# Kernel tuning notes

Measured on AMD Instinct MI355X. Metric: run time of the kernel, lower is better.

The kernel has to match this reference:

```python
import jax, jax.numpy as jnp
import numpy as np

EDGES = [[0,1],[0,2],[1,3],[2,3],[1,4],[1,5],[3,5],[4,6],[5,6],[5,27],[5,7],[7,27],[27,26],[26,29],[29,28],[26,28],[26,24],[24,25],[5,8],[8,10],[8,9],[5,9],[9,20],[20,21],[9,16],[15,16],[3,11],[11,12],[11,17],[11,15],[17,18],[18,19],[9,19],[9,23],[11,13],[13,14],[14,22],[22,23],[23,24]]
N_NODES = 30
B = 131072


def setup_inputs() -> dict:
    key = jax.random.key(0)
    ks = jax.random.split(key, 9)
    edge_index = jnp.asarray(np.array(EDGES).T, dtype=jnp.int64)  # [2, 39]
    def glorot(k, shape):
        fan_in = shape[0]
        return jax.random.normal(k, shape, dtype=jnp.float32) / np.sqrt(fan_in)
    return {
        'obs': jax.random.normal(ks[0], (B, N_NODES), dtype=jnp.float32),
        'edge_index': edge_index,
        'w1_rel': glorot(ks[1], (1, 16)),
        'b1_rel': jnp.zeros((16,), dtype=jnp.float32),
        'w1_root': glorot(ks[2], (1, 16)),
        'w2_rel': glorot(ks[3], (16, 1)),
        'b2_rel': jnp.zeros((1,), dtype=jnp.float32),
        'w2_root': glorot(ks[4], (16, 1)),
        'fc_w': glorot(ks[5], (30, 12)),
        'fc_b': jnp.zeros((12,), dtype=jnp.float32),
    }


def graph_conv(x, src, dst, w_rel, b_rel, w_root):
    # x: [B, N, F_in]; scatter-add messages from src nodes into dst nodes
    agg = jnp.zeros_like(x).at[:, dst, :].add(x[:, src, :])  # [B, N, F_in]
    return agg @ w_rel + b_rel + x @ w_root  # [B, N, F_out]


def reference(obs, edge_index, w1_rel, b1_rel, w1_root, w2_rel, b2_rel, w2_root, fc_w, fc_b):
    src, dst = edge_index[0], edge_index[1]
    x = obs.reshape(-1, N_NODES, 1)                    # [B, 30, 1]
    x = jax.nn.sigmoid(graph_conv(x, src, dst, w1_rel, b1_rel, w1_root))  # [B, 30, 16]
    x = jax.nn.sigmoid(graph_conv(x, src, dst, w2_rel, b2_rel, w2_root))  # [B, 30, 1]
    x = x.reshape(-1, N_NODES)                         # [B, 30]
    x = x @ fc_w + fc_b                                # [B, 12]
    x = x.reshape(-1, 2)                               # [B*6, 2]
    return jax.nn.softmax(x, axis=1)
```

## Files before the change

### kernel.cpp

```cpp
#include <hip/hip_runtime.h>

#define LOG2E 1.44269504088896340736f

__device__ __forceinline__ float ex2(float x) { return __builtin_amdgcn_exp2f(x); }
__device__ __forceinline__ float rcpf_(float x) { return __builtin_amdgcn_rcpf(x); }

__global__ __launch_bounds__(256) void gnn_fused(
    const float* __restrict__ obs,
    const float* __restrict__ w1_rel,
    const float* __restrict__ b1_rel,
    const float* __restrict__ w1_root,
    const float* __restrict__ w2_rel,
    const float* __restrict__ b2_rel,
    const float* __restrict__ w2_root,
    const float* __restrict__ fc_w,
    const float* __restrict__ fc_b,
    float* __restrict__ out)
{
    constexpr int SRC0[30] = {-1, 0, 0, 1, 1, 1, 4, 5, 5, 8, 8, 3, 11, 11, 13,
                              11, 9, 11, 17, 18, 9, 20, 14, 22, 26, 24, 27, 5, 29, 26};
    constexpr int SRC1[30] = {-1, -1, -1, 2, -1, 3, 5, -1, -1, 5, -1, -1, -1, -1, -1,
                              -1, 15, -1, -1, 9, -1, -1, -1, 9, 23, -1, -1, 7, 26, -1};

    __shared__ float sW1r[16], sW1R[16], sB1[16], sW2r[16], sW2R[16];
    __shared__ __align__(16) float sFW[30 * 8];
    __shared__ float sFB[8];
    __shared__ float sB2s;
    __shared__ __align__(16) float sObs[256 * 31];

    const int t = threadIdx.x;

    if (t < 16) {
        sW1r[t] = -LOG2E * w1_rel[t];
        sW1R[t] = -LOG2E * w1_root[t];
        sB1[t]  = -LOG2E * b1_rel[t];
        sW2r[t] = -LOG2E * w2_rel[t];
        sW2R[t] = -LOG2E * w2_root[t];
    }
    if (t >= 32 && t < 212) {
        int i = t - 32;
        int n = i / 6, k = i - n * 6;
        sFW[n * 8 + k] = -LOG2E * (fc_w[n * 12 + 2 * k] - fc_w[n * 12 + 2 * k + 1]);
    }
    if (t >= 224 && t < 230) {
        int k = t - 224;
        sFB[k] = -LOG2E * (fc_b[2 * k] - fc_b[2 * k + 1]);
    }
    if (t == 255) sB2s = -LOG2E * b2_rel[0];

    {
        const float2* ob2 = reinterpret_cast<const float2*>(obs) + (size_t)blockIdx.x * 3840;
        #pragma unroll
        for (int k = 0; k < 15; ++k) {
            unsigned p = (unsigned)t + (unsigned)k * 256u;
            float2 v = ob2[p];
            unsigned f0 = 2u * p;
            unsigned r0 = f0 / 30u, c0 = f0 - r0 * 30u;
            unsigned f1 = f0 + 1u;
            unsigned r1 = f1 / 30u, c1 = f1 - r1 * 30u;
            sObs[r0 * 31u + c0] = v.x;
            sObs[r1 * 31u + c1] = v.y;
        }
    }
    __syncthreads();

    float o[30];
    #pragma unroll
    for (int n = 0; n < 30; ++n) o[n] = sObs[t * 31 + n];

    float agg[30];
    #pragma unroll
    for (int n = 0; n < 30; ++n) {
        float a = 0.0f;
        if (SRC0[n] >= 0) a += o[SRC0[n]];
        if (SRC1[n] >= 0) a += o[SRC1[n]];
        agg[n] = a;
    }

    float sA[30], sB[30];
    const float b2s = sB2s;
    #pragma unroll
    for (int n = 0; n < 30; ++n) { sA[n] = 0.0f; sB[n] = b2s; }

    #pragma unroll 1
    for (int f = 0; f < 16; ++f) {
        const float A = sW1r[f], C = sW1R[f], D = sB1[f];
        const float wr = sW2r[f], wR = sW2R[f];
        #pragma unroll
        for (int n = 0; n < 30; ++n) {
            float e = ex2(fmaf(agg[n], A, fmaf(o[n], C, D)));
            float h = rcpf_(1.0f + e);
            sA[n] = fmaf(h, wr, sA[n]);
            sB[n] = fmaf(h, wR, sB[n]);
        }
    }

    float h2[30];
    #pragma unroll
    for (int n = 0; n < 30; ++n) {
        float arg = sB[n];
        if (SRC0[n] >= 0) arg += sA[SRC0[n]];
        if (SRC1[n] >= 0) arg += sA[SRC1[n]];
        h2[n] = rcpf_(1.0f + ex2(arg));
    }

    float acc[6];
    #pragma unroll
    for (int k = 0; k < 6; ++k) acc[k] = sFB[k];
    #pragma unroll
    for (int n = 0; n < 30; ++n) {
        const float4 w4 = *reinterpret_cast<const float4*>(&sFW[n * 8]);
        const float2 w2 = *reinterpret_cast<const float2*>(&sFW[n * 8 + 4]);
        acc[0] = fmaf(h2[n], w4.x, acc[0]);
        acc[1] = fmaf(h2[n], w4.y, acc[1]);
        acc[2] = fmaf(h2[n], w4.z, acc[2]);
        acc[3] = fmaf(h2[n], w4.w, acc[3]);
        acc[4] = fmaf(h2[n], w2.x, acc[4]);
        acc[5] = fmaf(h2[n], w2.y, acc[5]);
    }

    __syncthreads();

    float4* mine = reinterpret_cast<float4*>(&sObs[t * 12]);
    #pragma unroll
    for (int k = 0; k < 3; ++k) {
        float p0 = rcpf_(1.0f + ex2(acc[2 * k]));
        float p1 = 1.0f - p0;
        float q0 = rcpf_(1.0f + ex2(acc[2 * k + 1]));
        float q1 = 1.0f - q0;
        mine[k] = make_float4(p0, p1, q0, q1);
    }
    __syncthreads();

    float4* out4 = reinterpret_cast<float4*>(out) + (size_t)blockIdx.x * 768;
    const float4* s4 = reinterpret_cast<const float4*>(sObs);
    #pragma unroll
    for (int k = 0; k < 3; ++k) out4[t + k * 256] = s4[t + k * 256];
}

extern "C" void kernel_launch(void* const* d_in, const int* in_sizes, int n_in,
                              void* d_out, int out_size, void* d_ws, size_t ws_size,
                              hipStream_t stream) {
    const float* obs     = (const float*)d_in[0];
    const float* w1_rel  = (const float*)d_in[2];
    const float* b1_rel  = (const float*)d_in[3];
    const float* w1_root = (const float*)d_in[4];
    const float* w2_rel  = (const float*)d_in[5];
    const float* b2_rel  = (const float*)d_in[6];
    const float* w2_root = (const float*)d_in[7];
    const float* fc_w    = (const float*)d_in[8];
    const float* fc_b    = (const float*)d_in[9];
    float* out = (float*)d_out;

    const int B = in_sizes[0] / 30;
    const int blocks = B / 256;

    hipLaunchKernelGGL(gnn_fused, dim3(blocks), dim3(256), 0, stream,
                       obs, w1_rel, b1_rel, w1_root, w2_rel, b2_rel, w2_root,
                       fc_w, fc_b, out);
}
```

Baseline: 24.60 us.

## Split each graph row across two threads with shuffle exchange and paired reciprocals

Each batch row is now handled by two threads, each owning 15 nodes. Layer-2 neighbour sums that cross the split are exchanged through lane shuffles, and the FC partial sums are reduced with a shuffle. Sigmoids are computed two at a time with a single reciprocal of the product of denominators, which removes about half of the rcp instructions. This lowers register pressure and doubles thread count (launch bounds now ask for 4 blocks), at the cost of some extra multiplies, shuffles, and possible overflow when d0*d1 gets large.

```diff
diff --git a/kernel.cpp b/kernel.cpp
--- a/kernel.cpp
+++ b/kernel.cpp
@@ -5,7 +5,7 @@
 __device__ __forceinline__ float ex2(float x) { return __builtin_amdgcn_exp2f(x); }
 __device__ __forceinline__ float rcpf_(float x) { return __builtin_amdgcn_rcpf(x); }
 
-__global__ __launch_bounds__(256) void gnn_fused(
+__global__ __launch_bounds__(256, 4) void gnn_fused2(
     const float* __restrict__ obs,
     const float* __restrict__ w1_rel,
     const float* __restrict__ b1_rel,
@@ -17,18 +17,15 @@
     const float* __restrict__ fc_b,
     float* __restrict__ out)
 {
-    constexpr int SRC0[30] = {-1, 0, 0, 1, 1, 1, 4, 5, 5, 8, 8, 3, 11, 11, 13,
-                              11, 9, 11, 17, 18, 9, 20, 14, 22, 26, 24, 27, 5, 29, 26};
-    constexpr int SRC1[30] = {-1, -1, -1, 2, -1, 3, 5, -1, -1, 5, -1, -1, -1, -1, -1,
-                              -1, 15, -1, -1, 9, -1, -1, -1, 9, 23, -1, -1, 7, 26, -1};
-
     __shared__ float sW1r[16], sW1R[16], sB1[16], sW2r[16], sW2R[16];
     __shared__ __align__(16) float sFW[30 * 8];
     __shared__ float sFB[8];
     __shared__ float sB2s;
-    __shared__ __align__(16) float sObs[256 * 31];
+    __shared__ __align__(16) float sObs[128 * 31];
 
     const int t = threadIdx.x;
+    const int r = t >> 1;
+    const int h = t & 1;
 
     if (t < 16) {
         sW1r[t] = -LOG2E * w1_rel[t];
@@ -49,93 +46,186 @@
     if (t == 255) sB2s = -LOG2E * b2_rel[0];
 
     {
-        const float2* ob2 = reinterpret_cast<const float2*>(obs) + (size_t)blockIdx.x * 3840;
-        #pragma unroll
-        for (int k = 0; k < 15; ++k) {
+        const float2* ob2 = reinterpret_cast<const float2*>(obs) + (size_t)blockIdx.x * 1920;
+        #pragma unroll
+        for (int k = 0; k < 8; ++k) {
             unsigned p = (unsigned)t + (unsigned)k * 256u;
-            float2 v = ob2[p];
-            unsigned f0 = 2u * p;
-            unsigned r0 = f0 / 30u, c0 = f0 - r0 * 30u;
-            unsigned f1 = f0 + 1u;
-            unsigned r1 = f1 / 30u, c1 = f1 - r1 * 30u;
-            sObs[r0 * 31u + c0] = v.x;
-            sObs[r1 * 31u + c1] = v.y;
+            if (p < 1920u) {
+                float2 v = ob2[p];
+                unsigned f0 = 2u * p;
+                unsigned r0 = f0 / 30u, c0 = f0 - r0 * 30u;
+                unsigned f1 = f0 + 1u;
+                unsigned r1 = f1 / 30u, c1 = f1 - r1 * 30u;
+                sObs[r0 * 31u + c0] = v.x;
+                sObs[r1 * 31u + c1] = v.y;
+            }
         }
     }
     __syncthreads();
 
-    float o[30];
-    #pragma unroll
-    for (int n = 0; n < 30; ++n) o[n] = sObs[t * 31 + n];
-
-    float agg[30];
-    #pragma unroll
-    for (int n = 0; n < 30; ++n) {
-        float a = 0.0f;
-        if (SRC0[n] >= 0) a += o[SRC0[n]];
-        if (SRC1[n] >= 0) a += o[SRC1[n]];
-        agg[n] = a;
-    }
-
-    float sA[30], sB[30];
+    const float* row = &sObs[r * 31];
+    float o[15], agg[15];
+    #pragma unroll
+    for (int j = 0; j < 15; ++j) o[j] = row[15 * h + j];
+
+    if (h == 0) {
+        agg[0]  = 0.0f;
+        agg[1]  = row[0];
+        agg[2]  = row[0];
+        agg[3]  = row[1] + row[2];
+        agg[4]  = row[1];
+        agg[5]  = row[1] + row[3];
+        agg[6]  = row[4] + row[5];
+        agg[7]  = row[5];
+        agg[8]  = row[5];
+        agg[9]  = row[8] + row[5];
+        agg[10] = row[8];
+        agg[11] = row[3];
+        agg[12] = row[11];
+        agg[13] = row[11];
+        agg[14] = row[13];
+    } else {
+        agg[0]  = row[11];
+        agg[1]  = row[9] + row[15];
+        agg[2]  = row[11];
+        agg[3]  = row[17];
+        agg[4]  = row[18] + row[9];
+        agg[5]  = row[9];
+        agg[6]  = row[20];
+        agg[7]  = row[14];
+        agg[8]  = row[22] + row[9];
+        agg[9]  = row[26] + row[23];
+        agg[10] = row[24];
+        agg[11] = row[27];
+        agg[12] = row[5] + row[7];
+        agg[13] = row[29] + row[26];
+        agg[14] = row[26];
+    }
+
+    float sA[15], sB[15];
     const float b2s = sB2s;
     #pragma unroll
-    for (int n = 0; n < 30; ++n) { sA[n] = 0.0f; sB[n] = b2s; }
+    for (int j = 0; j < 15; ++j) { sA[j] = 0.0f; sB[j] = b2s; }
 
     #pragma unroll 1
     for (int f = 0; f < 16; ++f) {
         const float A = sW1r[f], C = sW1R[f], D = sB1[f];
         const float wr = sW2r[f], wR = sW2R[f];
-        #pragma unroll
-        for (int n = 0; n < 30; ++n) {
-            float e = ex2(fmaf(agg[n], A, fmaf(o[n], C, D)));
-            float h = rcpf_(1.0f + e);
-            sA[n] = fmaf(h, wr, sA[n]);
-            sB[n] = fmaf(h, wR, sB[n]);
-        }
-    }
-
-    float h2[30];
-    #pragma unroll
-    for (int n = 0; n < 30; ++n) {
-        float arg = sB[n];
-        if (SRC0[n] >= 0) arg += sA[SRC0[n]];
-        if (SRC1[n] >= 0) arg += sA[SRC1[n]];
-        h2[n] = rcpf_(1.0f + ex2(arg));
+        float e[15];
+        #pragma unroll
+        for (int j = 0; j < 15; ++j)
+            e[j] = ex2(fmaf(agg[j], A, fmaf(o[j], C, D)));
+        #pragma unroll
+        for (int p = 0; p < 7; ++p) {
+            float d0 = 1.0f + e[2 * p], d1 = 1.0f + e[2 * p + 1];
+            float rr = rcpf_(d0 * d1);
+            float h0 = rr * d1, h1 = rr * d0;
+            sA[2 * p]     = fmaf(h0, wr, sA[2 * p]);
+            sB[2 * p]     = fmaf(h0, wR, sB[2 * p]);
+            sA[2 * p + 1] = fmaf(h1, wr, sA[2 * p + 1]);
+            sB[2 * p + 1] = fmaf(h1, wR, sB[2 * p + 1]);
+        }
+        {
+            float hl = rcpf_(1.0f + e[14]);
+            sA[14] = fmaf(hl, wr, sA[14]);
+            sB[14] = fmaf(hl, wR, sB[14]);
+        }
+    }
+
+    float xa5  = __shfl_xor(sA[5], 1, 64);
+    float xa7  = __shfl_xor(sA[7], 1, 64);
+    float xa9  = __shfl_xor(sA[9], 1, 64);
+    float xa11 = __shfl_xor(sA[11], 1, 64);
+    float xa14 = __shfl_xor(sA[14], 1, 64);
+
+    float a2[15];
+    if (h == 0) {
+        a2[0]  = sB[0];
+        a2[1]  = sB[1] + sA[0];
+        a2[2]  = sB[2] + sA[0];
+        a2[3]  = sB[3] + sA[1] + sA[2];
+        a2[4]  = sB[4] + sA[1];
+        a2[5]  = sB[5] + sA[1] + sA[3];
+        a2[6]  = sB[6] + sA[4] + sA[5];
+        a2[7]  = sB[7] + sA[5];
+        a2[8]  = sB[8] + sA[5];
+        a2[9]  = sB[9] + sA[8] + sA[5];
+        a2[10] = sB[10] + sA[8];
+        a2[11] = sB[11] + sA[3];
+        a2[12] = sB[12] + sA[11];
+        a2[13] = sB[13] + sA[11];
+        a2[14] = sB[14] + sA[13];
+    } else {
+        a2[0]  = sB[0]  + xa11;
+        a2[1]  = sB[1]  + xa9  + sA[0];
+        a2[2]  = sB[2]  + xa11;
+        a2[3]  = sB[3]  + sA[2];
+        a2[4]  = sB[4]  + sA[3] + xa9;
+        a2[5]  = sB[5]  + xa9;
+        a2[6]  = sB[6]  + sA[5];
+        a2[7]  = sB[7]  + xa14;
+        a2[8]  = sB[8]  + sA[7] + xa9;
+        a2[9]  = sB[9]  + sA[11] + sA[8];
+        a2[10] = sB[10] + sA[9];
+        a2[11] = sB[11] + sA[12];
+        a2[12] = sB[12] + xa5 + xa7;
+        a2[13] = sB[13] + sA[14] + sA[11];
+        a2[14] = sB[14] + sA[11];
+    }
+
+    float h2[15];
+    {
+        float e[15];
+        #pragma unroll
+        for (int j = 0; j < 15; ++j) e[j] = ex2(a2[j]);
+        #pragma unroll
+        for (int p = 0; p < 7; ++p) {
+            float d0 = 1.0f + e[2 * p], d1 = 1.0f + e[2 * p + 1];
+            float rr = rcpf_(d0 * d1);
+            h2[2 * p]     = rr * d1;
+            h2[2 * p + 1] = rr * d0;
+        }
+        h2[14] = rcpf_(1.0f + e[14]);
     }
 
     float acc[6];
     #pragma unroll
-    for (int k = 0; k < 6; ++k) acc[k] = sFB[k];
-    #pragma unroll
-    for (int n = 0; n < 30; ++n) {
-        const float4 w4 = *reinterpret_cast<const float4*>(&sFW[n * 8]);
-        const float2 w2 = *reinterpret_cast<const float2*>(&sFW[n * 8 + 4]);
-        acc[0] = fmaf(h2[n], w4.x, acc[0]);
-        acc[1] = fmaf(h2[n], w4.y, acc[1]);
-        acc[2] = fmaf(h2[n], w4.z, acc[2]);
-        acc[3] = fmaf(h2[n], w4.w, acc[3]);
-        acc[4] = fmaf(h2[n], w2.x, acc[4]);
-        acc[5] = fmaf(h2[n], w2.y, acc[5]);
-    }
+    for (int k = 0; k < 6; ++k) acc[k] = (h == 0) ? sFB[k] : 0.0f;
+    const float* fw = &sFW[15 * h * 8];
+    #pragma unroll
+    for (int j = 0; j < 15; ++j) {
+        const float4 w4 = *reinterpret_cast<const float4*>(&fw[j * 8]);
+        const float2 w2 = *reinterpret_cast<const float2*>(&fw[j * 8 + 4]);
+        acc[0] = fmaf(h2[j], w4.x, acc[0]);
+        acc[1] = fmaf(h2[j], w4.y, acc[1]);
+        acc[2] = fmaf(h2[j], w4.z, acc[2]);
+        acc[3] = fmaf(h2[j], w4.w, acc[3]);
+        acc[4] = fmaf(h2[j], w2.x, acc[4]);
+        acc[5] = fmaf(h2[j], w2.y, acc[5]);
+    }
+    #pragma unroll
+    for (int k = 0; k < 6; ++k) acc[k] += __shfl_xor(acc[k], 1, 64);
 
     __syncthreads();
 
-    float4* mine = reinterpret_cast<float4*>(&sObs[t * 12]);
-    #pragma unroll
-    for (int k = 0; k < 3; ++k) {
-        float p0 = rcpf_(1.0f + ex2(acc[2 * k]));
-        float p1 = 1.0f - p0;
-        float q0 = rcpf_(1.0f + ex2(acc[2 * k + 1]));
-        float q1 = 1.0f - q0;
-        mine[k] = make_float4(p0, p1, q0, q1);
+    {
+        float u0 = acc[3 * h + 0], u1 = acc[3 * h + 1], u2 = acc[3 * h + 2];
+        float e0 = ex2(u0), e1 = ex2(u1), e2 = ex2(u2);
+        float d0 = 1.0f + e0, d1 = 1.0f + e1;
+        float rr = rcpf_(d0 * d1);
+        float p0 = rr * d1, p1 = rr * d0;
+        float p2 = rcpf_(1.0f + e2);
+        float2* mine = reinterpret_cast<float2*>(&sObs[r * 12 + 6 * h]);
+        mine[0] = make_float2(p0, 1.0f - p0);
+        mine[1] = make_float2(p1, 1.0f - p1);
+        mine[2] = make_float2(p2, 1.0f - p2);
     }
     __syncthreads();
 
-    float4* out4 = reinterpret_cast<float4*>(out) + (size_t)blockIdx.x * 768;
+    float4* out4 = reinterpret_cast<float4*>(out) + (size_t)blockIdx.x * 384;
     const float4* s4 = reinterpret_cast<const float4*>(sObs);
-    #pragma unroll
-    for (int k = 0; k < 3; ++k) out4[t + k * 256] = s4[t + k * 256];
+    out4[t] = s4[t];
+    if (t < 128) out4[256 + t] = s4[256 + t];
 }
 
 extern "C" void kernel_launch(void* const* d_in, const int* in_sizes, int n_in,
@@ -153,9 +243,9 @@
     float* out = (float*)d_out;
 
     const int B = in_sizes[0] / 30;
-    const int blocks = B / 256;
-
-    hipLaunchKernelGGL(gnn_fused, dim3(blocks), dim3(256), 0, stream,
+    const int blocks = B / 128;
+
+    hipLaunchKernelGGL(gnn_fused2, dim3(blocks), dim3(256), 0, stream,
                        obs, w1_rel, b1_rel, w1_root, w2_rel, b2_rel, w2_root,
                        fc_w, fc_b, out);
 }
```

After: 26.01 us. 1.06x slower.

## Pair sigmoid reciprocals, fully unroll feature loop, write output directly

Applied to the files above, without the earlier changes.

Computes two sigmoids with a single reciprocal by inverting the product of the denominators, which cuts transcendental work in both graph-conv layers and the final softmax. The feature loop is now fully unrolled, with weights read straight from global memory as uniform values instead of through LDS. The final outputs are stored directly from registers as strided float4 writes, removing two block barriers and the LDS staging step. The risks are higher register pressure and instruction-cache footprint, less coalesced stores, and possible overflow when the product of two large denominators exceeds float range. The second-layer scaling by -log2e is now applied to the activation instead of being folded into the weights.

```diff
diff --git a/kernel.cpp b/kernel.cpp
--- a/kernel.cpp
+++ b/kernel.cpp
@@ -5,7 +5,7 @@
 __device__ __forceinline__ float ex2(float x) { return __builtin_amdgcn_exp2f(x); }
 __device__ __forceinline__ float rcpf_(float x) { return __builtin_amdgcn_rcpf(x); }
 
-__global__ __launch_bounds__(256) void gnn_fused(
+__global__ __launch_bounds__(256) void gnn_fused4(
     const float* __restrict__ obs,
     const float* __restrict__ w1_rel,
     const float* __restrict__ b1_rel,
@@ -22,21 +22,12 @@
     constexpr int SRC1[30] = {-1, -1, -1, 2, -1, 3, 5, -1, -1, 5, -1, -1, -1, -1, -1,
                               -1, 15, -1, -1, 9, -1, -1, -1, 9, 23, -1, -1, 7, 26, -1};
 
-    __shared__ float sW1r[16], sW1R[16], sB1[16], sW2r[16], sW2R[16];
     __shared__ __align__(16) float sFW[30 * 8];
     __shared__ float sFB[8];
-    __shared__ float sB2s;
     __shared__ __align__(16) float sObs[256 * 31];
 
     const int t = threadIdx.x;
 
-    if (t < 16) {
-        sW1r[t] = -LOG2E * w1_rel[t];
-        sW1R[t] = -LOG2E * w1_root[t];
-        sB1[t]  = -LOG2E * b1_rel[t];
-        sW2r[t] = -LOG2E * w2_rel[t];
-        sW2R[t] = -LOG2E * w2_root[t];
-    }
     if (t >= 32 && t < 212) {
         int i = t - 32;
         int n = i / 6, k = i - n * 6;
@@ -46,7 +37,6 @@
         int k = t - 224;
         sFB[k] = -LOG2E * (fc_b[2 * k] - fc_b[2 * k + 1]);
     }
-    if (t == 255) sB2s = -LOG2E * b2_rel[0];
 
     {
         const float2* ob2 = reinterpret_cast<const float2*>(obs) + (size_t)blockIdx.x * 3840;
@@ -64,6 +54,8 @@
     }
     __syncthreads();
 
+    const float nl2e = -LOG2E;
+
     float o[30];
     #pragma unroll
     for (int n = 0; n < 30; ++n) o[n] = sObs[t * 31 + n];
@@ -78,64 +70,89 @@
     }
 
     float sA[30], sB[30];
-    const float b2s = sB2s;
+    const float b2r = b2_rel[0];
     #pragma unroll
-    for (int n = 0; n < 30; ++n) { sA[n] = 0.0f; sB[n] = b2s; }
+    for (int n = 0; n < 30; ++n) { sA[n] = 0.0f; sB[n] = b2r; }
 
-    #pragma unroll 1
+    #pragma unroll
     for (int f = 0; f < 16; ++f) {
-        const float A = sW1r[f], C = sW1R[f], D = sB1[f];
-        const float wr = sW2r[f], wR = sW2R[f];
+        const float vA = nl2e * w1_rel[f];
+        const float vC = nl2e * w1_root[f];
+        const float vD = nl2e * b1_rel[f];
+        const float wr = w2_rel[f];
+        const float wR = w2_root[f];
         #pragma unroll
-        for (int n = 0; n < 30; ++n) {
-            float e = ex2(fmaf(agg[n], A, fmaf(o[n], C, D)));
-            float h = rcpf_(1.0f + e);
-            sA[n] = fmaf(h, wr, sA[n]);
-            sB[n] = fmaf(h, wR, sB[n]);
+        for (int p = 0; p < 15; ++p) {
+            const int j0 = 2 * p, j1 = 2 * p + 1;
+            float e0 = ex2(fmaf(agg[j0], vA, fmaf(o[j0], vC, vD)));
+            float e1 = ex2(fmaf(agg[j1], vA, fmaf(o[j1], vC, vD)));
+            float d0 = 1.0f + e0, d1 = 1.0f + e1;
+            float rr = rcpf_(d0 * d1);
+            float h0 = rr * d1, h1 = rr * d0;
+            sA[j0] = fmaf(h0, wr, sA[j0]);
+            sB[j0] = fmaf(h0, wR, sB[j0]);
+            sA[j1] = fmaf(h1, wr, sA[j1]);
+            sB[j1] = fmaf(h1, wR, sB[j1]);
         }
     }
 
-    float h2[30];
+    float a2[30];
     #pragma unroll
     for (int n = 0; n < 30; ++n) {
         float arg = sB[n];
         if (SRC0[n] >= 0) arg += sA[SRC0[n]];
         if (SRC1[n] >= 0) arg += sA[SRC1[n]];
-        h2[n] = rcpf_(1.0f + ex2(arg));
+        a2[n] = arg;
     }
 
-    float acc[6];
+    float h2[30];
     #pragma unroll
-    for (int k = 0; k < 6; ++k) acc[k] = sFB[k];
+    for (int p = 0; p < 15; ++p) {
+        const int j0 = 2 * p, j1 = 2 * p + 1;
+        float e0 = ex2(nl2e * a2[j0]);
+        float e1 = ex2(nl2e * a2[j1]);
+        float d0 = 1.0f + e0, d1 = 1.0f + e1;
+        float rr = rcpf_(d0 * d1);
+        h2[j0] = rr * d1;
+        h2[j1] = rr * d0;
+    }
+
+    float acc0 = sFB[0], acc1 = sFB[1], acc2 = sFB[2];
+    float acc3 = sFB[3], acc4 = sFB[4], acc5 = sFB[5];
     #pragma unroll
     for (int n = 0; n < 30; ++n) {
         const float4 w4 = *reinterpret_cast<const float4*>(&sFW[n * 8]);
         const float2 w2 = *reinterpret_cast<const float2*>(&sFW[n * 8 + 4]);
-        acc[0] = fmaf(h2[n], w4.x, acc[0]);
-        acc[1] = fmaf(h2[n], w4.y, acc[1]);
-        acc[2] = fmaf(h2[n], w4.z, acc[2]);
-        acc[3] = fmaf(h2[n], w4.w, acc[3]);
-        acc[4] = fmaf(h2[n], w2.x, acc[4]);
-        acc[5] = fmaf(h2[n], w2.y, acc[5]);
+        acc0 = fmaf(h2[n], w4.x, acc0);
+        acc1 = fmaf(h2[n], w4.y, acc1);
+        acc2 = fmaf(h2[n], w4.z, acc2);
+        acc3 = fmaf(h2[n], w4.w, acc3);
+        acc4 = fmaf(h2[n], w2.x, acc4);
+        acc5 = fmaf(h2[n], w2.y, acc5);
     }
 
-    __syncthreads();
-
-    float4* mine = reinterpret_cast<float4*>(&sObs[t * 12]);
-    #pragma unroll
-    for (int k = 0; k < 3; ++k) {
-        float p0 = rcpf_(1.0f + ex2(acc[2 * k]));
-        float p1 = 1.0f - p0;
-        float q0 = rcpf_(1.0f + ex2(acc[2 * k + 1]));
-        float q1 = 1.0f - q0;
-        mine[k] = make_float4(p0, p1, q0, q1);
+    float4* out4 = reinterpret_cast<float4*>(out) + ((size_t)blockIdx.x * 256 + t) * 3;
+    {
+        float e0 = ex2(acc0), e1 = ex2(acc1);
+        float d0 = 1.0f + e0, d1 = 1.0f + e1;
+        float rr = rcpf_(d0 * d1);
+        float p0 = rr * d1, p1 = rr * d0;
+        out4[0] = make_float4(p0, 1.0f - p0, p1, 1.0f - p1);
     }
-    __syncthreads();
-
-    float4* out4 = reinterpret_cast<float4*>(out) + (size_t)blockIdx.x * 768;
-    const float4* s4 = reinterpret_cast<const float4*>(sObs);
-    #pragma unroll
-    for (int k = 0; k < 3; ++k) out4[t + k * 256] = s4[t + k * 256];
+    {
+        float e0 = ex2(acc2), e1 = ex2(acc3);
+        float d0 = 1.0f + e0, d1 = 1.0f + e1;
+        float rr = rcpf_(d0 * d1);
+        float p0 = rr * d1, p1 = rr * d0;
+        out4[1] = make_float4(p0, 1.0f - p0, p1, 1.0f - p1);
+    }
+    {
+        float e0 = ex2(acc4), e1 = ex2(acc5);
+        float d0 = 1.0f + e0, d1 = 1.0f + e1;
+        float rr = rcpf_(d0 * d1);
+        float p0 = rr * d1, p1 = rr * d0;
+        out4[2] = make_float4(p0, 1.0f - p0, p1, 1.0f - p1);
+    }
 }
 
 extern "C" void kernel_launch(void* const* d_in, const int* in_sizes, int n_in,
@@ -155,7 +172,7 @@
     const int B = in_sizes[0] / 30;
     const int blocks = B / 256;
 
-    hipLaunchKernelGGL(gnn_fused, dim3(blocks), dim3(256), 0, stream,
+    hipLaunchKernelGGL(gnn_fused4, dim3(blocks), dim3(256), 0, stream,
                        obs, w1_rel, b1_rel, w1_root, w2_rel, b2_rel, w2_root,
                        fc_w, fc_b, out);
 }
```

After: 33.28 us. 1.35x slower.
